# Performance work log

Measured on AMD Instinct MI355X. Metric: run time of the kernel, lower is better.

The kernel has to match this reference:

```python
import jax, jax.numpy as jnp
import numpy as np

EMBED_DIMS = 1024
NUM_HEADS = 16
HEAD_DIMS = EMBED_DIMS // NUM_HEADS


def setup_inputs() -> dict:
    key = jax.random.key(0)
    k_x, k_wqkv, k_bqkv, k_wp, k_bp = jax.random.split(key, 5)
    B, N, D = 2, 2048, EMBED_DIMS
    x = jax.random.normal(k_x, (B, N, D), dtype=jnp.float32)
    # torch nn.Linear(in, out): weight [out, in], y = x @ W.T + b
    s = 1.0 / np.sqrt(D)
    W_qkv = jax.random.uniform(k_wqkv, (3 * D, D), jnp.float32, -s, s)
    b_qkv = jax.random.uniform(k_bqkv, (3 * D,), jnp.float32, -s, s)
    W_proj = jax.random.uniform(k_wp, (D, D), jnp.float32, -s, s)
    b_proj = jax.random.uniform(k_bp, (D,), jnp.float32, -s, s)
    return {"x": x, "W_qkv": W_qkv, "b_qkv": b_qkv, "W_proj": W_proj, "b_proj": b_proj}


def reference(x, W_qkv, b_qkv, W_proj, b_proj):
    B, N, D = x.shape
    H, Hd = NUM_HEADS, HEAD_DIMS
    # qkv projection: [B, N, 3, H, Hd] -> split q, k, v as [B, H, N, Hd]
    qkv = (x @ W_qkv.T + b_qkv).reshape(B, N, 3, H, Hd).transpose(2, 0, 3, 1, 4)
    q, k, v = qkv[0], qkv[1], qkv[2]
    scale = 1.0 / jnp.sqrt(jnp.asarray(Hd, x.dtype))
    attn = jnp.einsum("bhqd,bhkd->bhqk", q, k) * scale  # [B, H, N, N]
    attn = jax.nn.softmax(attn, axis=-1)
    out = jnp.einsum("bhqk,bhkd->bhqd", attn, v)  # [B, H, N, Hd]
    out = out.transpose(0, 2, 1, 3).reshape(B, N, D)
    out = out @ W_proj.T + b_proj
    return out
```

## Files before the change

kernel.cpp:

```cpp
#include <hip/hip_runtime.h>

typedef _Float16 f16x8 __attribute__((ext_vector_type(8)));
typedef __attribute__((ext_vector_type(4))) float f32x4;

static __device__ __forceinline__ unsigned short f2h(float f) {
  return __builtin_bit_cast(unsigned short, (_Float16)f);
}

#if __has_builtin(__builtin_amdgcn_exp2f)
#define EXP2(x) __builtin_amdgcn_exp2f(x)
#else
#define EXP2(x) exp2f(x)
#endif

#define GLOAD_LDS16(gp, lp)                                          \
  __builtin_amdgcn_global_load_lds(                                  \
      (const __attribute__((address_space(1))) unsigned int*)(gp),   \
      (__attribute__((address_space(3))) unsigned int*)(lp), 16, 0, 0)

__global__ __launch_bounds__(256) void cvt_all(
    const float* __restrict__ X, const float* __restrict__ Wq,
    const float* __restrict__ Wp, unsigned short* __restrict__ Xb,
    unsigned short* __restrict__ Wqb, unsigned short* __restrict__ Wpb) {
  const int i = blockIdx.x * 256 + threadIdx.x;
  const float4* src;
  unsigned short* dst;
  int off;
  if (i < 1048576) {
    src = (const float4*)X; dst = Xb; off = i;
  } else if (i < 1835008) {
    src = (const float4*)Wq; dst = Wqb; off = i - 1048576;
  } else {
    src = (const float4*)Wp; dst = Wpb; off = i - 1835008;
  }
  const float4 v = src[off];
  *(ushort4*)(dst + (size_t)off * 4) =
      make_ushort4(f2h(v.x), f2h(v.y), f2h(v.z), f2h(v.w));
}

__global__ __launch_bounds__(256, 3) void qkv_gemm(
    const unsigned short* __restrict__ Xb, const unsigned short* __restrict__ Wb,
    const float* __restrict__ bias, unsigned short* __restrict__ Qb,
    unsigned short* __restrict__ Kb, unsigned short* __restrict__ Vt) {
  __shared__ __align__(16) unsigned short A_sh[2][128 * 32];
  __shared__ __align__(16) unsigned short B_sh[2][128 * 32];
  const int n0 = blockIdx.x * 128, m0 = blockIdx.y * 128;
  const int tid = threadIdx.x, lane = tid & 63, wave = tid >> 6;
  const int wr = wave >> 1, wc = wave & 1;
  const int lm = lane & 15, lg = lane >> 4;
  const int r4 = lane >> 2;
  const int sg8 = (((lane & 3) ^ ((r4 >> 1) & 3)) * 8);
  const int lgx = (lg ^ ((lm >> 1) & 3)) * 8;

  f32x4 acc[4][4] = {};

#define QSTAGE(k0_, b_)                                                       \
  do {                                                                        \
    _Pragma("unroll")                                                         \
    for (int j = 0; j < 2; ++j) {                                             \
      const int chunk = wave * 2 + j;                                         \
      const int row = chunk * 16 + r4;                                        \
      GLOAD_LDS16(Xb + (size_t)(m0 + row) * 1024 + (k0_) + sg8,               \
                  &A_sh[b_][chunk * 512]);                                    \
      GLOAD_LDS16(Wb + (size_t)(n0 + row) * 1024 + (k0_) + sg8,               \
                  &B_sh[b_][chunk * 512]);                                    \
    }                                                                         \
  } while (0)

  QSTAGE(0, 0);

  for (int it = 0; it < 32; ++it) {
    const int cur = it & 1;
    __syncthreads();
    if (it < 31) QSTAGE((it + 1) * 32, cur ^ 1);

    f16x8 af[4], bfr[4];
#pragma unroll
    for (int mi = 0; mi < 4; ++mi)
      af[mi] = *(const f16x8*)&A_sh[cur][(wr * 64 + mi * 16 + lm) * 32 + lgx];
#pragma unroll
    for (int ni = 0; ni < 4; ++ni)
      bfr[ni] = *(const f16x8*)&B_sh[cur][(wc * 64 + ni * 16 + lm) * 32 + lgx];
    __builtin_amdgcn_s_setprio(1);
#pragma unroll
    for (int mi = 0; mi < 4; ++mi)
#pragma unroll
      for (int ni = 0; ni < 4; ++ni)
        acc[mi][ni] = __builtin_amdgcn_mfma_f32_16x16x32_f16(
            af[mi], bfr[ni], acc[mi][ni], 0, 0, 0);
    __builtin_amdgcn_s_setprio(0);
  }
#undef QSTAGE

  const float qscale = 0.18033688011112042f;
#pragma unroll
  for (int mi = 0; mi < 4; ++mi) {
#pragma unroll
    for (int ni = 0; ni < 4; ++ni) {
      const int gn = n0 + wc * 64 + ni * 16 + lm;
      const float bv = bias[gn];
      const int which = gn >> 10;
      const int h = (gn >> 6) & 15;
      const int hd = gn & 63;
      float v[4];
#pragma unroll
      for (int r = 0; r < 4; ++r) v[r] = acc[mi][ni][r] + bv;
      const int gm0 = m0 + wr * 64 + mi * 16 + lg * 4;
      const int bb = gm0 >> 11;
      const int nq0 = gm0 & 2047;
      if (which == 0) {
        unsigned short* p = Qb + (((size_t)bb * 16 + h) * 2048 + nq0) * 64 + hd;
        p[0] = f2h(v[0] * qscale);   p[64] = f2h(v[1] * qscale);
        p[128] = f2h(v[2] * qscale); p[192] = f2h(v[3] * qscale);
      } else if (which == 1) {
        unsigned short* p = Kb + (((size_t)bb * 16 + h) * 2048 + nq0) * 64 + hd;
        p[0] = f2h(v[0]);   p[64] = f2h(v[1]);
        p[128] = f2h(v[2]); p[192] = f2h(v[3]);
      } else {
        *(ushort4*)(Vt + (((size_t)bb * 16 + h) * 64 + hd) * 2048 + nq0) =
            make_ushort4(f2h(v[0]), f2h(v[1]), f2h(v[2]), f2h(v[3]));
      }
    }
  }
}

__global__ __launch_bounds__(512) void attn_kernel(
    const unsigned short* __restrict__ Qb, const unsigned short* __restrict__ Kb,
    const unsigned short* __restrict__ Vt, unsigned short* __restrict__ Ob) {
  __shared__ __align__(16) unsigned short K_sh[2][2][64 * 32];
  __shared__ __align__(16) unsigned short V_sh[2][2][64 * 32];
  __shared__ __align__(16) unsigned short P_sh[128 * 68];
  const int bh = blockIdx.y, q0 = blockIdx.x * 128;
  const size_t base = (size_t)bh * (2048 * 64);
  const unsigned short* Qp = Qb + base;
  const unsigned short* Kp = Kb + base;
  const unsigned short* Vp = Vt + base;
  const int tid = threadIdx.x, lane = tid & 63, wave = tid >> 6;
  const int lm = lane & 15, lg = lane >> 4;
  const int r4 = lane >> 2;
  const int sg8 = (((lane & 3) ^ ((r4 >> 1) & 3)) * 8);
  const int lgx = (lg ^ ((lm >> 1) & 3)) * 8;

  f16x8 qf[2];
#pragma unroll
  for (int kc = 0; kc < 2; ++kc)
    qf[kc] = *(const f16x8*)(Qp +
        (size_t)(q0 + wave * 16 + lm) * 64 + kc * 32 + lg * 8);

  f32x4 o[4] = {};
  float lsum[4] = {};

  const bool isV = wave >= 4;
  const int plane = wave & 1;
  const int half = (wave >> 1) & 1;

#define STAGE(kt_, b_)                                                        \
  do {                                                                        \
    if (!isV) {                                                               \
      _Pragma("unroll")                                                       \
      for (int qv = 0; qv < 2; ++qv)                                          \
        GLOAD_LDS16(Kp + (size_t)((kt_) * 64 + half * 32 + qv * 16 + r4) * 64 \
                        + plane * 32 + sg8,                                   \
                    &K_sh[b_][plane][(half * 2 + qv) * 512]);                 \
    } else {                                                                  \
      _Pragma("unroll")                                                       \
      for (int qv = 0; qv < 2; ++qv)                                          \
        GLOAD_LDS16(Vp + (size_t)(half * 32 + qv * 16 + r4) * 2048 +          \
                        (kt_) * 64 + plane * 32 + sg8,                        \
                    &V_sh[b_][plane][(half * 2 + qv) * 512]);                 \
    }                                                                         \
  } while (0)

  STAGE(0, 0);

  for (int kt = 0; kt < 32; ++kt) {
    const int cur = kt & 1;
    __syncthreads();
    if (kt < 31) STAGE(kt + 1, cur ^ 1);

    f32x4 s[4] = {};
#pragma unroll
    for (int kc = 0; kc < 2; ++kc) {
#pragma unroll
      for (int ni = 0; ni < 4; ++ni) {
        const f16x8 kf =
            *(const f16x8*)&K_sh[cur][kc][(ni * 16 + lm) * 32 + lgx];
        s[ni] = __builtin_amdgcn_mfma_f32_16x16x32_f16(qf[kc], kf, s[ni], 0, 0, 0);
      }
    }

#pragma unroll
    for (int ni = 0; ni < 4; ++ni) {
      float p0 = EXP2(s[ni][0]), p1 = EXP2(s[ni][1]);
      float p2 = EXP2(s[ni][2]), p3 = EXP2(s[ni][3]);
      lsum[0] += p0; lsum[1] += p1; lsum[2] += p2; lsum[3] += p3;
      unsigned short* pp = &P_sh[(wave * 16 + lg * 4) * 68 + ni * 16 + lm];
      pp[0] = f2h(p0);    pp[68] = f2h(p1);
      pp[136] = f2h(p2);  pp[204] = f2h(p3);
    }

#pragma unroll
    for (int kc = 0; kc < 2; ++kc) {
      const f16x8 pa =
          *(const f16x8*)&P_sh[(wave * 16 + lm) * 68 + kc * 32 + lg * 8];
#pragma unroll
      for (int ni = 0; ni < 4; ++ni) {
        const f16x8 vb =
            *(const f16x8*)&V_sh[cur][kc][(ni * 16 + lm) * 32 + lgx];
        o[ni] = __builtin_amdgcn_mfma_f32_16x16x32_f16(pa, vb, o[ni], 0, 0, 0);
      }
    }
  }
#undef STAGE

  const int b = bh >> 4, h = bh & 15;
#pragma unroll
  for (int r = 0; r < 4; ++r) {
    float l = lsum[r];
    l += __shfl_xor(l, 1);
    l += __shfl_xor(l, 2);
    l += __shfl_xor(l, 4);
    l += __shfl_xor(l, 8);
    const float inv = 1.0f / l;
    const int nq = q0 + wave * 16 + lg * 4 + r;
    unsigned short* p = Ob + ((size_t)(b * 2048 + nq) * 16 + h) * 64 + lm;
    p[0] = f2h(o[0][r] * inv);
    p[16] = f2h(o[1][r] * inv);
    p[32] = f2h(o[2][r] * inv);
    p[48] = f2h(o[3][r] * inv);
  }
}

__global__ __launch_bounds__(256) void proj_gemm(
    const unsigned short* __restrict__ A, const unsigned short* __restrict__ Wb,
    const float* __restrict__ bias, float* __restrict__ Out) {
  __shared__ __align__(16) unsigned short A_sh[2][64 * 32];
  __shared__ __align__(16) unsigned short B_sh[2][128 * 32];
  const int n0 = blockIdx.x * 128, m0 = blockIdx.y * 64;
  const int tid = threadIdx.x, lane = tid & 63, wave = tid >> 6;
  const int wr = wave >> 1, wc = wave & 1, lm = lane & 15, lg = lane >> 4;
  const int r4 = lane >> 2;
  const int sg8 = (((lane & 3) ^ ((r4 >> 1) & 3)) * 8);
  const int lgx = (lg ^ ((lm >> 1) & 3)) * 8;

  f32x4 acc[2][4] = {};

#define PSTAGE(k0_, b_)                                                       \
  do {                                                                        \
    {                                                                         \
      const int row = wave * 16 + r4;                                         \
      GLOAD_LDS16(A + (size_t)(m0 + row) * 1024 + (k0_) + sg8,                \
                  &A_sh[b_][wave * 512]);                                     \
    }                                                                         \
    _Pragma("unroll")                                                         \
    for (int j = 0; j < 2; ++j) {                                             \
      const int chunk = wave * 2 + j;                                         \
      const int row = chunk * 16 + r4;                                        \
      GLOAD_LDS16(Wb + (size_t)(n0 + row) * 1024 + (k0_) + sg8,               \
                  &B_sh[b_][chunk * 512]);                                    \
    }                                                                         \
  } while (0)

  PSTAGE(0, 0);

  for (int it = 0; it < 32; ++it) {
    const int cur = it & 1;
    __syncthreads();
    if (it < 31) PSTAGE((it + 1) * 32, cur ^ 1);

    f16x8 af[2], bfr[4];
#pragma unroll
    for (int mi = 0; mi < 2; ++mi)
      af[mi] = *(const f16x8*)&A_sh[cur][(wr * 32 + mi * 16 + lm) * 32 + lgx];
#pragma unroll
    for (int ni = 0; ni < 4; ++ni)
      bfr[ni] = *(const f16x8*)&B_sh[cur][(wc * 64 + ni * 16 + lm) * 32 + lgx];
#pragma unroll
    for (int mi = 0; mi < 2; ++mi)
#pragma unroll
      for (int ni = 0; ni < 4; ++ni)
        acc[mi][ni] = __builtin_amdgcn_mfma_f32_16x16x32_f16(
            af[mi], bfr[ni], acc[mi][ni], 0, 0, 0);
  }
#undef PSTAGE

#pragma unroll
  for (int mi = 0; mi < 2; ++mi)
#pragma unroll
    for (int ni = 0; ni < 4; ++ni) {
      const int gn = n0 + wc * 64 + ni * 16 + lm;
      const float bv = bias[gn];
#pragma unroll
      for (int r = 0; r < 4; ++r) {
        const int gm = m0 + wr * 32 + mi * 16 + lg * 4 + r;
        Out[(size_t)gm * 1024 + gn] = acc[mi][ni][r] + bv;
      }
    }
}

extern "C" void kernel_launch(void* const* d_in, const int* in_sizes, int n_in,
                              void* d_out, int out_size, void* d_ws, size_t ws_size,
                              hipStream_t stream) {
  const float* x      = (const float*)d_in[0];
  const float* W_qkv  = (const float*)d_in[1];
  const float* b_qkv  = (const float*)d_in[2];
  const float* W_proj = (const float*)d_in[3];
  const float* b_proj = (const float*)d_in[4];
  float* out = (float*)d_out;

  unsigned short* Qb  = (unsigned short*)d_ws;
  unsigned short* Kb  = Qb + 4194304;
  unsigned short* Vt  = Kb + 4194304;
  unsigned short* Ao  = Vt + 4194304;
  unsigned short* Xb  = Ao + 4194304;
  unsigned short* Wqb = Xb + 4194304;
  unsigned short* Wpb = Wqb + 3145728;

  cvt_all<<<8192, 256, 0, stream>>>(x, W_qkv, W_proj, Xb, Wqb, Wpb);
  qkv_gemm<<<dim3(24, 32), 256, 0, stream>>>(Xb, Wqb, b_qkv, Qb, Kb, Vt);
  attn_kernel<<<dim3(16, 32), 512, 0, stream>>>(Qb, Kb, Vt, Ao);
  proj_gemm<<<dim3(8, 64), 256, 0, stream>>>(Ao, Wpb, b_proj, out);
}
```

Measured before the change: 194.4 us.

## Keep softmax probabilities in registers via transposed QK MFMA and permlane swaps

Swaps the MFMA operand order so the score tile comes out transposed, with each lane holding key-consecutive values for one query row. The fp16 probabilities are then packed and redistributed across lanes with permlane32/permlane16 swaps to form the A operand of the PV MFMA, which removes the P_sh shared-memory round trip and its bank traffic. Row sums become a single per-lane accumulator reduced across lane groups at the end, and launch bounds request 4 blocks per CU to raise occupancy. This relies on the permlane swap layout exactly matching the MFMA operand layout, and adds cross-lane instructions in exchange for fewer LDS writes and reads.

```diff
diff --git a/kernel.cpp b/kernel.cpp
--- a/kernel.cpp
+++ b/kernel.cpp
@@ -5,6 +5,10 @@
 
 static __device__ __forceinline__ unsigned short f2h(float f) {
   return __builtin_bit_cast(unsigned short, (_Float16)f);
+}
+
+static __device__ __forceinline__ unsigned int pk2(float a, float b) {
+  return (unsigned int)f2h(a) | ((unsigned int)f2h(b) << 16);
 }
 
 #if __has_builtin(__builtin_amdgcn_exp2f)
@@ -124,12 +128,11 @@
   }
 }
 
-__global__ __launch_bounds__(512) void attn_kernel(
+__global__ __launch_bounds__(512, 4) void attn_kernel(
     const unsigned short* __restrict__ Qb, const unsigned short* __restrict__ Kb,
     const unsigned short* __restrict__ Vt, unsigned short* __restrict__ Ob) {
   __shared__ __align__(16) unsigned short K_sh[2][2][64 * 32];
   __shared__ __align__(16) unsigned short V_sh[2][2][64 * 32];
-  __shared__ __align__(16) unsigned short P_sh[128 * 68];
   const int bh = blockIdx.y, q0 = blockIdx.x * 128;
   const size_t base = (size_t)bh * (2048 * 64);
   const unsigned short* Qp = Qb + base;
@@ -148,7 +151,7 @@
         (size_t)(q0 + wave * 16 + lm) * 64 + kc * 32 + lg * 8);
 
   f32x4 o[4] = {};
-  float lsum[4] = {};
+  float lsum = 0.0f;
 
   const bool isV = wave >= 4;
   const int plane = wave & 1;
@@ -185,43 +188,51 @@
       for (int ni = 0; ni < 4; ++ni) {
         const f16x8 kf =
             *(const f16x8*)&K_sh[cur][kc][(ni * 16 + lm) * 32 + lgx];
-        s[ni] = __builtin_amdgcn_mfma_f32_16x16x32_f16(qf[kc], kf, s[ni], 0, 0, 0);
+        s[ni] = __builtin_amdgcn_mfma_f32_16x16x32_f16(kf, qf[kc], s[ni], 0, 0, 0);
       }
     }
 
+    unsigned int Wp_[4][2];
 #pragma unroll
     for (int ni = 0; ni < 4; ++ni) {
-      float p0 = EXP2(s[ni][0]), p1 = EXP2(s[ni][1]);
-      float p2 = EXP2(s[ni][2]), p3 = EXP2(s[ni][3]);
-      lsum[0] += p0; lsum[1] += p1; lsum[2] += p2; lsum[3] += p3;
-      unsigned short* pp = &P_sh[(wave * 16 + lg * 4) * 68 + ni * 16 + lm];
-      pp[0] = f2h(p0);    pp[68] = f2h(p1);
-      pp[136] = f2h(p2);  pp[204] = f2h(p3);
+      const float p0 = EXP2(s[ni][0]), p1 = EXP2(s[ni][1]);
+      const float p2 = EXP2(s[ni][2]), p3 = EXP2(s[ni][3]);
+      lsum += (p0 + p1) + (p2 + p3);
+      Wp_[ni][0] = pk2(p0, p1);
+      Wp_[ni][1] = pk2(p2, p3);
     }
 
 #pragma unroll
     for (int kc = 0; kc < 2; ++kc) {
-      const f16x8 pa =
-          *(const f16x8*)&P_sh[(wave * 16 + lm) * 68 + kc * 32 + lg * 8];
+      auto t0 = __builtin_amdgcn_permlane32_swap(Wp_[2 * kc][0], Wp_[2 * kc + 1][0],
+                                                 false, false);
+      auto u0 = __builtin_amdgcn_permlane16_swap(t0[0], t0[1], false, false);
+      auto t1 = __builtin_amdgcn_permlane32_swap(Wp_[2 * kc][1], Wp_[2 * kc + 1][1],
+                                                 false, false);
+      auto u1 = __builtin_amdgcn_permlane16_swap(t1[0], t1[1], false, false);
+      union { unsigned int u[4]; f16x8 v; } pa;
+      pa.u[0] = u0[0];
+      pa.u[1] = u1[0];
+      pa.u[2] = u0[1];
+      pa.u[3] = u1[1];
 #pragma unroll
       for (int ni = 0; ni < 4; ++ni) {
         const f16x8 vb =
             *(const f16x8*)&V_sh[cur][kc][(ni * 16 + lm) * 32 + lgx];
-        o[ni] = __builtin_amdgcn_mfma_f32_16x16x32_f16(pa, vb, o[ni], 0, 0, 0);
+        o[ni] = __builtin_amdgcn_mfma_f32_16x16x32_f16(pa.v, vb, o[ni], 0, 0, 0);
       }
     }
   }
 #undef STAGE
 
+  float total = lsum;
+  total += __shfl_xor(total, 16);
+  total += __shfl_xor(total, 32);
+
   const int b = bh >> 4, h = bh & 15;
 #pragma unroll
   for (int r = 0; r < 4; ++r) {
-    float l = lsum[r];
-    l += __shfl_xor(l, 1);
-    l += __shfl_xor(l, 2);
-    l += __shfl_xor(l, 4);
-    l += __shfl_xor(l, 8);
-    const float inv = 1.0f / l;
+    const float inv = 1.0f / __shfl(total, (lane & 48) | (lg * 4 + r));
     const int nq = q0 + wave * 16 + lg * 4 + r;
     unsigned short* p = Ob + ((size_t)(b * 2048 + nq) * 16 + h) * 64 + lm;
     p[0] = f2h(o[0][r] * inv);
```

Result: no change. 193.0 us (-0.7%).
